# Kernel optimization log

Hardware: AMD Instinct MI355X
Metric: run time of the kernel (lower is better)

## Reference

```python
import jax, jax.numpy as jnp
import numpy as np

WIN = (8, 8)
DIM = 256
HEADS = 8
B = 2048
NW = 64


def _make_buffers(win):
    wh, ww = win
    # relative_position_bias_table: (1, 2wh-1, 2ww-1, 2)
    rh = np.arange(-(wh - 1), wh, dtype=np.float32)
    rw = np.arange(-(ww - 1), ww, dtype=np.float32)
    gh, gw = np.meshgrid(rh, rw, indexing='ij')
    tbl = np.stack([gh, gw], axis=-1)[None]  # (1, 2wh-1, 2ww-1, 2)
    tbl[..., 0] /= (wh - 1)
    tbl[..., 1] /= (ww - 1)
    tbl *= 3.2
    tbl = np.sign(tbl) * (1.0 - np.exp(-np.abs(tbl)))
    # relative_position_index: (n, n)
    ch, cw = np.meshgrid(np.arange(wh), np.arange(ww), indexing='ij')
    cf = np.stack([ch.reshape(-1), cw.reshape(-1)])  # (2, n)
    rel = cf[:, :, None] - cf[:, None, :]            # (2, n, n)
    rel = rel.transpose(1, 2, 0).astype(np.int64)
    rel[..., 0] += wh - 1
    rel[..., 1] += ww - 1
    rel[..., 0] *= 2 * ww - 1
    rpi = rel.sum(-1).astype(np.int32)
    return jnp.asarray(tbl, dtype=jnp.float32), jnp.asarray(rpi)


def setup_inputs() -> dict:
    key = jax.random.key(0)
    ks = jax.random.split(key, 12)
    c2 = DIM // 2
    n = WIN[0] * WIN[1]
    s = 0.02
    inp = {
        'x': jax.random.normal(ks[0], (B, n, DIM), dtype=jnp.float32),
        'mask': jax.random.normal(ks[1], (NW, n, n), dtype=jnp.float32),
        'qw': jax.random.normal(ks[2], (2, c2, c2), dtype=jnp.float32) * s,
        'qb': jnp.zeros((2, c2), dtype=jnp.float32),
        'kw': jax.random.normal(ks[3], (2, c2, c2), dtype=jnp.float32) * s,
        'kb': jnp.zeros((2, c2), dtype=jnp.float32),
        'vw': jax.random.normal(ks[4], (2, c2, c2), dtype=jnp.float32) * s,
        'vb': jnp.zeros((2, c2), dtype=jnp.float32),
        'pw': jax.random.normal(ks[5], (2, c2, c2), dtype=jnp.float32) * s,
        'pb': jnp.zeros((2, c2), dtype=jnp.float32),
        'mlp_w1': jax.random.normal(ks[6], (2, 128), dtype=jnp.float32) * s,
        'mlp_b1': jnp.zeros((128,), dtype=jnp.float32),
        'mlp_w2': jax.random.normal(ks[7], (128, HEADS), dtype=jnp.float32) * s,
        'logit_scale': jnp.full((HEADS, 1, 1), np.log(10.0), dtype=jnp.float32),
    }
    tbl, rpi = _make_buffers(WIN)
    inp['rpb_table'] = tbl
    inp['rpi'] = rpi
    return inp


def _l2norm(v, eps=1e-12):
    nrm = jnp.sqrt(jnp.sum(v * v, axis=-1, keepdims=True))
    return v / jnp.maximum(nrm, eps)


def _forward(x, mask, qw, qb, kw, kb, vw, vb, pw, pb,
             mlp_w1, mlp_b1, mlp_w2, logit_scale, rpb_table, rpi):
    b, n, c = x.shape
    h = logit_scale.shape[0]
    c2 = c // 2
    hd = c // h
    xb = x.reshape(b, n, 2, c2)  # branch split on channel halves

    def dual(w, bias):  # residual dual-branch linear: xb + Linear(xb)
        return xb + jnp.einsum('bnsc,scd->bnsd', xb, w) + bias

    # (b, n, 2, c2) -> (b, n, c) -> (b, h, n, hd)
    q = dual(qw, qb).reshape(b, n, h, hd).transpose(0, 2, 1, 3)
    k = dual(kw, kb).reshape(b, n, h, hd).transpose(0, 2, 1, 3)
    v = dual(vw, vb).reshape(b, n, h, hd).transpose(0, 2, 1, 3)

    attn = jnp.einsum('bhnd,bhmd->bhnm', _l2norm(q), _l2norm(k))
    scale = jnp.exp(jnp.minimum(logit_scale, jnp.log(jnp.float32(100.0))))  # (h,1,1)
    attn = attn * scale[None]

    # CPB-MLP relative position bias
    hid = jax.nn.relu(rpb_table @ mlp_w1 + mlp_b1)         # (1, 2wh-1, 2ww-1, 128)
    tbl = (hid @ mlp_w2).reshape(-1, h)                    # ((2wh-1)(2ww-1), h)
    bias = tbl[rpi.reshape(-1)].reshape(n, n, h).transpose(2, 0, 1)
    attn = attn + 16.0 * jax.nn.sigmoid(bias)[None]

    if mask is not None:
        nw = mask.shape[0]
        attn = attn.reshape(b // nw, nw, h, n, n) + mask[None, :, None]
        attn = attn.reshape(b, h, n, n)

    attn = jax.nn.softmax(attn, axis=-1)
    out = jnp.einsum('bhnm,bhmd->bhnd', attn, v).transpose(0, 2, 1, 3).reshape(b, n, c)

    ob = out.reshape(b, n, 2, c2)
    y = jnp.einsum('bnsc,scd->bnsd', ob, pw) + pb
    return y.reshape(b, n, c)


def reference(x, mask, qw, qb, kw, kb, vw, vb, pw, pb,
              mlp_w1, mlp_b1, mlp_w2, logit_scale, rpb_table, rpi):
    return _forward(x, mask, qw, qb, kw, kb, vw, vb, pw, pb,
                    mlp_w1, mlp_b1, mlp_w2, logit_scale, rpb_table, rpi)
```

## Files before the change

### kernel.cpp

```cpp
#include <hip/hip_runtime.h>
#include <stdint.h>

#define B_    2048
#define N_    64
#define C_    256
#define C2_   128
#define H_    8
#define NW_   64
#define NPOS  225

typedef __attribute__((ext_vector_type(8))) short short8;
typedef __attribute__((ext_vector_type(4))) float float4v;

union U8 { unsigned u[4]; short8 s; };

__device__ float g_scale[H_];
__device__ float g_t8[NPOS][H_];
__device__ __align__(16) float g_sb[NW_ * H_ * N_ * N_];
__device__ unsigned short g_wt[4][2][C2_][C2_];

__device__ __forceinline__ float b2f(unsigned short u) {
  return __uint_as_float(((unsigned int)u) << 16);
}
__device__ __forceinline__ unsigned short f2b(float f) {
  unsigned int u = __float_as_uint(f);
  u += 0x7fffu + ((u >> 16) & 1u);
  return (unsigned short)(u >> 16);
}

__global__ __launch_bounds__(256) void k_prep1(
    const float* __restrict__ tbl, const float* __restrict__ w1,
    const float* __restrict__ b1, const float* __restrict__ w2,
    const float* __restrict__ ls) {
  __shared__ float sw1[256], sb1[128], sw2[1024];
  const int t = threadIdx.x;
  sw1[t] = w1[t];
  if (t < 128) sb1[t] = b1[t];
#pragma unroll
  for (int it = 0; it < 4; ++it) sw2[it * 256 + t] = w2[it * 256 + t];
  __syncthreads();
  if (t < NPOS) {
    float a0 = tbl[2 * t], a1 = tbl[2 * t + 1];
    float acc[H_];
#pragma unroll
    for (int h = 0; h < H_; ++h) acc[h] = 0.f;
    for (int j = 0; j < 128; ++j) {
      float hid = fmaxf(a0 * sw1[j] + a1 * sw1[128 + j] + sb1[j], 0.f);
#pragma unroll
      for (int h = 0; h < H_; ++h) acc[h] += hid * sw2[j * H_ + h];
    }
#pragma unroll
    for (int h = 0; h < H_; ++h) g_t8[t][h] = acc[h];
  }
  if (t < H_) g_scale[t] = __expf(fminf(ls[t], 4.6051702f));
}

__global__ __launch_bounds__(256) void k_prep2(
    const float* __restrict__ mask, const int* __restrict__ rpi) {
  const int base = blockIdx.x * 1024;
#pragma unroll
  for (int it = 0; it < 4; ++it) {
    int idx = base + it * 256 + threadIdx.x;
    int j  = idx & 63;
    int i  = (idx >> 6) & 63;
    int h  = (idx >> 12) & 7;
    int wd = idx >> 15;
    float v = g_t8[rpi[i * 64 + j]][h];
    g_sb[idx] = 16.f / (1.f + __expf(-v)) + mask[wd * 4096 + i * 64 + j];
  }
}

__global__ __launch_bounds__(256) void k_prepw(
    const float* __restrict__ qw, const float* __restrict__ kw,
    const float* __restrict__ vw, const float* __restrict__ pw) {
  __shared__ unsigned short lt[128 * 132];
  const int t = threadIdx.x;
  const int p = blockIdx.x >> 1, s = blockIdx.x & 1;
  const float* src = (p == 0 ? qw : p == 1 ? kw : p == 2 ? vw : pw) + s * (C2_ * C2_);
#pragma unroll
  for (int it = 0; it < 64; ++it) {
    int e = it * 256 + t;
    int c = e >> 7, d = e & 127;
    lt[d * 132 + c] = f2b(src[e]);
  }
  __syncthreads();
#pragma unroll
  for (int it = 0; it < 64; ++it) {
    int e = it * 256 + t;
    int d = e >> 7, c = e & 127;
    g_wt[p][s][d][c] = lt[d * 132 + c];
  }
}

__global__ __launch_bounds__(1024, 4) void k_main(
    const float* __restrict__ x, float* __restrict__ out,
    const float* __restrict__ qb, const float* __restrict__ kb,
    const float* __restrict__ vb, const float* __restrict__ pb) {
  __shared__ __align__(16) unsigned short xs[N_ * 264];
  __shared__ __align__(16) unsigned short qs[N_ * 264];
  __shared__ __align__(16) unsigned short ks[N_ * 264];
  __shared__ __align__(16) unsigned short vt[C_ * 72];

  const int t    = threadIdx.x;
  const int lane = t & 63;
  const int w    = __builtin_amdgcn_readfirstlane(t >> 6);
  const int b    = blockIdx.x;
  const int l15  = lane & 15;
  const int qd   = lane >> 4;

  {
    const float4* xg = (const float4*)(x + (size_t)b * (N_ * C_));
#pragma unroll
    for (int it = 0; it < 4; ++it) {
      int e = t + 1024 * it;
      int row = e >> 6, c4 = (e & 63) << 2;
      float4 v = xg[e];
      uint2 pk;
      pk.x = ((unsigned)f2b(v.y) << 16) | f2b(v.x);
      pk.y = ((unsigned)f2b(v.w) << 16) | f2b(v.z);
      *(uint2*)&xs[row * 264 + c4] = pk;
    }
  }
  __syncthreads();

  const int s1 = w >> 3;
  const int jls = (w >> 1) & 3;
  const int jl = 32 * jls;
  const int mh = w & 1;
  const float scl = g_scale[s1 * 4 + jls];
  for (int pj = 0; pj < 3; ++pj) {
    const float* bi = pj == 0 ? qb : (pj == 1 ? kb : vb);
    float4v acc[2][2];
    {
      float b0 = bi[s1 * C2_ + jl + l15], b1 = bi[s1 * C2_ + jl + 16 + l15];
#pragma unroll
      for (int mt = 0; mt < 2; ++mt) {
        acc[mt][0] = float4v{b0, b0, b0, b0};
        acc[mt][1] = float4v{b1, b1, b1, b1};
      }
    }
    const unsigned short* wt = &g_wt[pj][s1][0][0];
#pragma unroll
    for (int kc = 0; kc < 4; ++kc) {
      int ko = kc * 32 + qd * 8;
      short8 a[2], bf[2];
#pragma unroll
      for (int mt = 0; mt < 2; ++mt)
        a[mt] = *(const short8*)&xs[(32 * mh + mt * 16 + l15) * 264 + s1 * 128 + ko];
      bf[0] = *(const short8*)&wt[(jl + l15) * C2_ + ko];
      bf[1] = *(const short8*)&wt[(jl + 16 + l15) * C2_ + ko];
#pragma unroll
      for (int mt = 0; mt < 2; ++mt)
#pragma unroll
        for (int nt = 0; nt < 2; ++nt)
          acc[mt][nt] = __builtin_amdgcn_mfma_f32_16x16x32_bf16(
              a[mt], bf[nt], acc[mt][nt], 0, 0, 0);
    }
    unsigned short* dst = pj == 0 ? qs : ks;
#pragma unroll
    for (int mt = 0; mt < 2; ++mt) {
      int row0 = 32 * mh + mt * 16 + qd * 4;
      float vv[2][4];
#pragma unroll
      for (int nt = 0; nt < 2; ++nt)
#pragma unroll
        for (int r = 0; r < 4; ++r)
          vv[nt][r] = acc[mt][nt][r] +
                      b2f(xs[(row0 + r) * 264 + s1 * 128 + jl + nt * 16 + l15]);
      if (pj < 2) {
        float ss[4];
#pragma unroll
        for (int r = 0; r < 4; ++r) ss[r] = vv[0][r] * vv[0][r] + vv[1][r] * vv[1][r];
#pragma unroll
        for (int m = 1; m < 16; m <<= 1)
#pragma unroll
          for (int r = 0; r < 4; ++r) ss[r] += __shfl_xor(ss[r], m, 64);
#pragma unroll
        for (int r = 0; r < 4; ++r) {
          float rn = 1.0f / fmaxf(sqrtf(ss[r]), 1e-12f);
          if (pj == 0) rn *= scl;
          vv[0][r] *= rn;
          vv[1][r] *= rn;
        }
#pragma unroll
        for (int nt = 0; nt < 2; ++nt)
#pragma unroll
          for (int r = 0; r < 4; ++r)
            dst[(row0 + r) * 264 + s1 * 128 + jl + nt * 16 + l15] = f2b(vv[nt][r]);
      } else {
#pragma unroll
        for (int nt = 0; nt < 2; ++nt) {
          int chan = s1 * 128 + jl + nt * 16 + l15;
          uint2 pk;
          pk.x = ((unsigned)f2b(vv[nt][1]) << 16) | f2b(vv[nt][0]);
          pk.y = ((unsigned)f2b(vv[nt][3]) << 16) | f2b(vv[nt][2]);
          *(uint2*)&vt[chan * 72 + row0] = pk;
        }
      }
    }
  }
  __syncthreads();

  const int wm = w & 3, wg = w >> 2;
  const float* sbb = g_sb + (size_t)(b & 63) * (H_ * N_ * N_);
  const int hi_sel = lane & 32;
  const int src0 = l15 | ((((qd << 1) + 0) & 3) << 4);
  const int src1 = l15 | ((((qd << 1) + 1) & 3) << 4);
#pragma unroll
  for (int hh = 0; hh < 2; ++hh) {
    const int h = 2 * wg + hh;
    const float* sbh = sbb + h * 4096;
    short8 bq = *(const short8*)&qs[(16 * wm + l15) * 264 + h * 32 + qd * 8];
    float4v sacc[4];
#pragma unroll
    for (int nt = 0; nt < 4; ++nt) {
      float4 cv = *(const float4*)&sbh[(16 * wm + l15) * 64 + nt * 16 + qd * 4];
      float4v c = {cv.x, cv.y, cv.z, cv.w};
      short8 ak = *(const short8*)&ks[(nt * 16 + l15) * 264 + h * 32 + qd * 8];
      sacc[nt] = __builtin_amdgcn_mfma_f32_16x16x32_bf16(ak, bq, c, 0, 0, 0);
    }
    float e[4][4];
    float s = 0.f;
#pragma unroll
    for (int nt = 0; nt < 4; ++nt)
#pragma unroll
      for (int r = 0; r < 4; ++r) {
        e[nt][r] = __expf(sacc[nt][r]);
        s += e[nt][r];
      }
    s += __shfl_xor(s, 16, 64);
    s += __shfl_xor(s, 32, 64);
    float rr = 1.0f / s;
    unsigned pk[4][2];
#pragma unroll
    for (int nt = 0; nt < 4; ++nt)
#pragma unroll
      for (int rp = 0; rp < 2; ++rp)
        pk[nt][rp] = ((unsigned)f2b(e[nt][2 * rp + 1] * rr) << 16) |
                     f2b(e[nt][2 * rp] * rr);
    U8 au[2];
#pragma unroll
    for (int j2 = 0; j2 < 4; ++j2) {
      int src = (j2 >> 1) ? src1 : src0;
      int rp = j2 & 1;
      int r0 = __shfl((int)pk[0][rp], src, 64);
      int r1 = __shfl((int)pk[1][rp], src, 64);
      int r2 = __shfl((int)pk[2][rp], src, 64);
      int r3 = __shfl((int)pk[3][rp], src, 64);
      au[0].u[j2] = hi_sel ? (unsigned)r1 : (unsigned)r0;
      au[1].u[j2] = hi_sel ? (unsigned)r3 : (unsigned)r2;
    }
    float4v oacc[2];
    oacc[0] = float4v{0, 0, 0, 0};
    oacc[1] = float4v{0, 0, 0, 0};
#pragma unroll
    for (int kc = 0; kc < 2; ++kc) {
      short8 ap = au[kc].s;
#pragma unroll
      for (int nt2 = 0; nt2 < 2; ++nt2) {
        short8 bv = *(const short8*)&vt[(h * 32 + nt2 * 16 + l15) * 72 + kc * 32 + qd * 8];
        oacc[nt2] = __builtin_amdgcn_mfma_f32_16x16x32_bf16(ap, bv, oacc[nt2], 0, 0, 0);
      }
    }
#pragma unroll
    for (int nt2 = 0; nt2 < 2; ++nt2)
#pragma unroll
      for (int r = 0; r < 4; ++r)
        xs[(16 * wm + qd * 4 + r) * 264 + h * 32 + nt2 * 16 + l15] = f2b(oacc[nt2][r]);
  }
  __syncthreads();

  {
    float4v acc[2][2];
    float b0 = pb[s1 * C2_ + jl + l15], b1 = pb[s1 * C2_ + jl + 16 + l15];
#pragma unroll
    for (int mt = 0; mt < 2; ++mt) {
      acc[mt][0] = float4v{b0, b0, b0, b0};
      acc[mt][1] = float4v{b1, b1, b1, b1};
    }
    const unsigned short* wt = &g_wt[3][s1][0][0];
#pragma unroll
    for (int kc = 0; kc < 4; ++kc) {
      int ko = kc * 32 + qd * 8;
      short8 a[2], bf[2];
#pragma unroll
      for (int mt = 0; mt < 2; ++mt)
        a[mt] = *(const short8*)&xs[(32 * mh + mt * 16 + l15) * 264 + s1 * 128 + ko];
      bf[0] = *(const short8*)&wt[(jl + l15) * C2_ + ko];
      bf[1] = *(const short8*)&wt[(jl + 16 + l15) * C2_ + ko];
#pragma unroll
      for (int mt = 0; mt < 2; ++mt)
#pragma unroll
        for (int nt = 0; nt < 2; ++nt)
          acc[mt][nt] = __builtin_amdgcn_mfma_f32_16x16x32_bf16(
              a[mt], bf[nt], acc[mt][nt], 0, 0, 0);
    }
#pragma unroll
    for (int mt = 0; mt < 2; ++mt)
#pragma unroll
      for (int nt = 0; nt < 2; ++nt)
#pragma unroll
        for (int r = 0; r < 4; ++r)
          out[((size_t)b * N_ + 32 * mh + mt * 16 + qd * 4 + r) * C_ +
              s1 * 128 + jl + nt * 16 + l15] = acc[mt][nt][r];
  }
}

extern "C" void kernel_launch(void* const* d_in, const int* in_sizes, int n_in,
                              void* d_out, int out_size, void* d_ws, size_t ws_size,
                              hipStream_t stream) {
  const float* x    = (const float*)d_in[0];
  const float* mask = (const float*)d_in[1];
  const float* qw   = (const float*)d_in[2];
  const float* qb   = (const float*)d_in[3];
  const float* kw   = (const float*)d_in[4];
  const float* kb   = (const float*)d_in[5];
  const float* vw   = (const float*)d_in[6];
  const float* vb   = (const float*)d_in[7];
  const float* pw   = (const float*)d_in[8];
  const float* pb   = (const float*)d_in[9];
  const float* w1   = (const float*)d_in[10];
  const float* b1   = (const float*)d_in[11];
  const float* w2   = (const float*)d_in[12];
  const float* ls   = (const float*)d_in[13];
  const float* tbl  = (const float*)d_in[14];
  const int*   rpi  = (const int*)d_in[15];
  float* out = (float*)d_out;

  k_prep1<<<1, 256, 0, stream>>>(tbl, w1, b1, w2, ls);
  k_prep2<<<2048, 256, 0, stream>>>(mask, rpi);
  k_prepw<<<8, 256, 0, stream>>>(qw, kw, vw, pw);
  k_main<<<B_, 1024, 0, stream>>>(x, out, qb, kb, vb, pb);
}
```

Measured before the change: 421.0 us.

## Split each window across two blocks by channel half to cut LDS and block size

Each window is now handled by two 512-thread blocks, one per channel half and its four heads, instead of one 1024-thread block. Because the grouped projections and the per-head attention only touch their own half, each block stores only 128 channels in shared memory with a smaller row padding. This roughly halves per-block LDS and thread count, which should let more blocks reside per CU and improve latency hiding. In exchange, x rows are read as half-row strided segments, and the per-warp work in the attention phase is reorganised by query rows.

Result: faster. 391.9 us (-6.9%).

```diff
diff --git a/kernel.cpp b/kernel.cpp
--- a/kernel.cpp
+++ b/kernel.cpp
@@ -8,6 +8,8 @@
 #define H_    8
 #define NW_   64
 #define NPOS  225
+#define PX    136
+#define PV    72
 
 typedef __attribute__((ext_vector_type(8))) short short8;
 typedef __attribute__((ext_vector_type(4))) float float4v;
@@ -92,41 +94,42 @@
   }
 }
 
-__global__ __launch_bounds__(1024, 4) void k_main(
+__global__ __launch_bounds__(512) void k_main(
     const float* __restrict__ x, float* __restrict__ out,
     const float* __restrict__ qb, const float* __restrict__ kb,
     const float* __restrict__ vb, const float* __restrict__ pb) {
-  __shared__ __align__(16) unsigned short xs[N_ * 264];
-  __shared__ __align__(16) unsigned short qs[N_ * 264];
-  __shared__ __align__(16) unsigned short ks[N_ * 264];
-  __shared__ __align__(16) unsigned short vt[C_ * 72];
+  __shared__ __align__(16) unsigned short xs[N_ * PX];
+  __shared__ __align__(16) unsigned short qs[N_ * PX];
+  __shared__ __align__(16) unsigned short ks[N_ * PX];
+  __shared__ __align__(16) unsigned short vt[C2_ * PV];
 
   const int t    = threadIdx.x;
   const int lane = t & 63;
   const int w    = __builtin_amdgcn_readfirstlane(t >> 6);
-  const int b    = blockIdx.x;
+  const int bs   = blockIdx.x;
+  const int b    = bs >> 1;
+  const int s1   = bs & 1;
   const int l15  = lane & 15;
   const int qd   = lane >> 4;
 
   {
-    const float4* xg = (const float4*)(x + (size_t)b * (N_ * C_));
+    const float* xg = x + (size_t)b * (N_ * C_) + s1 * C2_;
 #pragma unroll
     for (int it = 0; it < 4; ++it) {
-      int e = t + 1024 * it;
-      int row = e >> 6, c4 = (e & 63) << 2;
-      float4 v = xg[e];
+      int e = t + 512 * it;
+      int row = e >> 5, c4 = (e & 31) << 2;
+      float4 v = *(const float4*)&xg[row * C_ + c4];
       uint2 pk;
       pk.x = ((unsigned)f2b(v.y) << 16) | f2b(v.x);
       pk.y = ((unsigned)f2b(v.w) << 16) | f2b(v.z);
-      *(uint2*)&xs[row * 264 + c4] = pk;
-    }
-  }
-  __syncthreads();
-
-  const int s1 = w >> 3;
-  const int jls = (w >> 1) & 3;
-  const int jl = 32 * jls;
-  const int mh = w & 1;
+      *(uint2*)&xs[row * PX + c4] = pk;
+    }
+  }
+  __syncthreads();
+
+  const int jls = w >> 1;
+  const int jl  = 32 * jls;
+  const int mh  = w & 1;
   const float scl = g_scale[s1 * 4 + jls];
   for (int pj = 0; pj < 3; ++pj) {
     const float* bi = pj == 0 ? qb : (pj == 1 ? kb : vb);
@@ -146,7 +149,7 @@
       short8 a[2], bf[2];
 #pragma unroll
       for (int mt = 0; mt < 2; ++mt)
-        a[mt] = *(const short8*)&xs[(32 * mh + mt * 16 + l15) * 264 + s1 * 128 + ko];
+        a[mt] = *(const short8*)&xs[(32 * mh + mt * 16 + l15) * PX + ko];
       bf[0] = *(const short8*)&wt[(jl + l15) * C2_ + ko];
       bf[1] = *(const short8*)&wt[(jl + 16 + l15) * C2_ + ko];
 #pragma unroll
@@ -166,7 +169,7 @@
 #pragma unroll
         for (int r = 0; r < 4; ++r)
           vv[nt][r] = acc[mt][nt][r] +
-                      b2f(xs[(row0 + r) * 264 + s1 * 128 + jl + nt * 16 + l15]);
+                      b2f(xs[(row0 + r) * PX + jl + nt * 16 + l15]);
       if (pj < 2) {
         float ss[4];
 #pragma unroll
@@ -186,37 +189,38 @@
         for (int nt = 0; nt < 2; ++nt)
 #pragma unroll
           for (int r = 0; r < 4; ++r)
-            dst[(row0 + r) * 264 + s1 * 128 + jl + nt * 16 + l15] = f2b(vv[nt][r]);
+            dst[(row0 + r) * PX + jl + nt * 16 + l15] = f2b(vv[nt][r]);
       } else {
 #pragma unroll
         for (int nt = 0; nt < 2; ++nt) {
-          int chan = s1 * 128 + jl + nt * 16 + l15;
+          int chan = jl + nt * 16 + l15;
           uint2 pk;
           pk.x = ((unsigned)f2b(vv[nt][1]) << 16) | f2b(vv[nt][0]);
           pk.y = ((unsigned)f2b(vv[nt][3]) << 16) | f2b(vv[nt][2]);
-          *(uint2*)&vt[chan * 72 + row0] = pk;
+          *(uint2*)&vt[chan * PV + row0] = pk;
         }
       }
     }
   }
   __syncthreads();
 
-  const int wm = w & 3, wg = w >> 2;
-  const float* sbb = g_sb + (size_t)(b & 63) * (H_ * N_ * N_);
+  const int hl = w >> 1;
+  const int rh = w & 1;
+  const int h  = s1 * 4 + hl;
+  const float* sbh = g_sb + ((size_t)(b & 63) * H_ + h) * 4096;
   const int hi_sel = lane & 32;
   const int src0 = l15 | ((((qd << 1) + 0) & 3) << 4);
   const int src1 = l15 | ((((qd << 1) + 1) & 3) << 4);
 #pragma unroll
-  for (int hh = 0; hh < 2; ++hh) {
-    const int h = 2 * wg + hh;
-    const float* sbh = sbb + h * 4096;
-    short8 bq = *(const short8*)&qs[(16 * wm + l15) * 264 + h * 32 + qd * 8];
+  for (int mq = 0; mq < 2; ++mq) {
+    const int r0 = 32 * rh + 16 * mq;
+    short8 bq = *(const short8*)&qs[(r0 + l15) * PX + hl * 32 + qd * 8];
     float4v sacc[4];
 #pragma unroll
     for (int nt = 0; nt < 4; ++nt) {
-      float4 cv = *(const float4*)&sbh[(16 * wm + l15) * 64 + nt * 16 + qd * 4];
+      float4 cv = *(const float4*)&sbh[(r0 + l15) * 64 + nt * 16 + qd * 4];
       float4v c = {cv.x, cv.y, cv.z, cv.w};
-      short8 ak = *(const short8*)&ks[(nt * 16 + l15) * 264 + h * 32 + qd * 8];
+      short8 ak = *(const short8*)&ks[(nt * 16 + l15) * PX + hl * 32 + qd * 8];
       sacc[nt] = __builtin_amdgcn_mfma_f32_16x16x32_bf16(ak, bq, c, 0, 0, 0);
     }
     float e[4][4];
@@ -243,12 +247,12 @@
     for (int j2 = 0; j2 < 4; ++j2) {
       int src = (j2 >> 1) ? src1 : src0;
       int rp = j2 & 1;
-      int r0 = __shfl((int)pk[0][rp], src, 64);
-      int r1 = __shfl((int)pk[1][rp], src, 64);
-      int r2 = __shfl((int)pk[2][rp], src, 64);
-      int r3 = __shfl((int)pk[3][rp], src, 64);
-      au[0].u[j2] = hi_sel ? (unsigned)r1 : (unsigned)r0;
-      au[1].u[j2] = hi_sel ? (unsigned)r3 : (unsigned)r2;
+      int r0v = __shfl((int)pk[0][rp], src, 64);
+      int r1v = __shfl((int)pk[1][rp], src, 64);
+      int r2v = __shfl((int)pk[2][rp], src, 64);
+      int r3v = __shfl((int)pk[3][rp], src, 64);
+      au[0].u[j2] = hi_sel ? (unsigned)r1v : (unsigned)r0v;
+      au[1].u[j2] = hi_sel ? (unsigned)r3v : (unsigned)r2v;
     }
     float4v oacc[2];
     oacc[0] = float4v{0, 0, 0, 0};
@@ -258,7 +262,7 @@
       short8 ap = au[kc].s;
 #pragma unroll
       for (int nt2 = 0; nt2 < 2; ++nt2) {
-        short8 bv = *(const short8*)&vt[(h * 32 + nt2 * 16 + l15) * 72 + kc * 32 + qd * 8];
+        short8 bv = *(const short8*)&vt[(hl * 32 + nt2 * 16 + l15) * PV + kc * 32 + qd * 8];
         oacc[nt2] = __builtin_amdgcn_mfma_f32_16x16x32_bf16(ap, bv, oacc[nt2], 0, 0, 0);
       }
     }
@@ -266,7 +270,7 @@
     for (int nt2 = 0; nt2 < 2; ++nt2)
 #pragma unroll
       for (int r = 0; r < 4; ++r)
-        xs[(16 * wm + qd * 4 + r) * 264 + h * 32 + nt2 * 16 + l15] = f2b(oacc[nt2][r]);
+        xs[(r0 + qd * 4 + r) * PX + hl * 32 + nt2 * 16 + l15] = f2b(oacc[nt2][r]);
   }
   __syncthreads();
 
@@ -285,7 +289,7 @@
       short8 a[2], bf[2];
 #pragma unroll
       for (int mt = 0; mt < 2; ++mt)
-        a[mt] = *(const short8*)&xs[(32 * mh + mt * 16 + l15) * 264 + s1 * 128 + ko];
+        a[mt] = *(const short8*)&xs[(32 * mh + mt * 16 + l15) * PX + ko];
       bf[0] = *(const short8*)&wt[(jl + l15) * C2_ + ko];
       bf[1] = *(const short8*)&wt[(jl + 16 + l15) * C2_ + ko];
 #pragma unroll
@@ -302,7 +306,7 @@
 #pragma unroll
         for (int r = 0; r < 4; ++r)
           out[((size_t)b * N_ + 32 * mh + mt * 16 + qd * 4 + r) * C_ +
-              s1 * 128 + jl + nt * 16 + l15] = acc[mt][nt][r];
+              s1 * C2_ + jl + nt * 16 + l15] = acc[mt][nt][r];
   }
 }
 
@@ -330,5 +334,5 @@
   k_prep1<<<1, 256, 0, stream>>>(tbl, w1, b1, w2, ls);
   k_prep2<<<2048, 256, 0, stream>>>(mask, rpi);
   k_prepw<<<8, 256, 0, stream>>>(qw, kw, vw, pw);
-  k_main<<<B_, 1024, 0, stream>>>(x, out, qb, kb, vb, pb);
-}
+  k_main<<<B_ * 2, 512, 0, stream>>>(x, out, qb, kb, vb, pb);
+}
```
